# Optimization experiments

Hardware: AMD Instinct MI355X
Metric: run time of the kernel (lower is better)

The kernel has to match this reference:

```python
import jax, jax.numpy as jnp
import numpy as np


def setup_inputs() -> dict:
    key = jax.random.key(0)
    k1, k2, k3 = jax.random.split(key, 3)
    N, K, C, M = 16, 32768, 16, 128
    pred_boxes = jax.random.normal(k1, (N, K, 5), dtype=jnp.float32)
    pred_cls = jax.random.normal(k2, (N, K, C), dtype=jnp.float32)
    target = jax.random.uniform(k3, (N, M, 5), dtype=jnp.float32)
    return {"pred_boxes": pred_boxes, "pred_cls": pred_cls, "target": target}


def _losses(pred_boxes, pred_cls, target):
    N, K, _ = pred_boxes.shape
    M = target.shape[1]
    C = pred_cls.shape[2]
    mask = target.sum(axis=2) != 0                      # (N, M)
    maskf = mask.astype(pred_boxes.dtype)
    denom = maskf.sum()
    tboxes = target[..., 1:]                            # (N, M, 4) corners (x1,y1,x2,y2)
    tcls = target[..., 0].astype(jnp.int32)             # (N, M)
    pconf = pred_boxes[..., 4]                          # (N, K)
    pb = pred_boxes[..., :4]                            # (N, K, 4) (x, y, w, h)

    # pred corners (N, 1, K)
    p_x1 = pb[:, None, :, 0]
    p_y1 = pb[:, None, :, 1]
    p_x2 = (pb[..., 2] + pb[..., 0])[:, None, :]
    p_y2 = (pb[..., 3] + pb[..., 1])[:, None, :]
    # target corners (N, M, 1)
    t_x1 = tboxes[..., 0:1]
    t_y1 = tboxes[..., 1:2]
    t_x2 = tboxes[..., 2:3]
    t_y2 = tboxes[..., 3:4]

    ix1 = jnp.maximum(p_x1, t_x1)
    iy1 = jnp.maximum(p_y1, t_y1)
    ix2 = jnp.minimum(p_x2, t_x2)
    iy2 = jnp.minimum(p_y2, t_y2)
    inter = jnp.clip(ix2 - ix1 + 1, 0) * jnp.clip(iy2 - iy1 + 1, 0)   # (N, M, K)
    a1 = (p_x2 - p_x1 + 1) * (p_y2 - p_y1 + 1)
    a2 = (t_x2 - t_x1 + 1) * (t_y2 - t_y1 + 1)
    iou = inter / (a1 + a2 - inter + 1e-16)

    best = jnp.argmax(iou, axis=-1)                     # (N, M)
    best_idx = jnp.where(mask, best, 0)                 # masked targets keep index 0 (as torch init)

    best_pb = jnp.take_along_axis(pb, best_idx[..., None], axis=1)       # (N, M, 4)
    best_cls = jnp.take_along_axis(pred_cls, best_idx[..., None], axis=1)  # (N, M, C)
    # NOTE: faithful to original: conf gather indices are never updated -> always index 0
    conf_idx = jnp.zeros((N, M), dtype=jnp.int32)
    best_conf = jax.nn.sigmoid(jnp.take_along_axis(pconf, conf_idx, axis=1))  # (N, M)

    def masked_mean(v):
        return (v * maskf).sum() / denom

    logp = jax.nn.log_softmax(best_cls, axis=-1)
    ce = -jnp.take_along_axis(logp, tcls[..., None], axis=-1)[..., 0]
    loss_cls = masked_mean(ce)

    loss_x = masked_mean((best_pb[..., 0] - tboxes[..., 0]) ** 2)
    loss_y = masked_mean((best_pb[..., 1] - tboxes[..., 1]) ** 2)
    loss_w = masked_mean((best_pb[..., 2] - (tboxes[..., 2] - tboxes[..., 0])) ** 2)
    loss_h = masked_mean((best_pb[..., 3] - (tboxes[..., 3] - tboxes[..., 1])) ** 2)

    labels = (best_conf > 0.5).astype(best_conf.dtype)
    bce = -(labels * jnp.log(best_conf) + (1.0 - labels) * jnp.log(1.0 - best_conf))
    loss_conf = masked_mean(bce)

    loss = loss_cls + loss_x + loss_y + loss_w + loss_h + loss_conf
    return loss, loss_cls, loss_x, loss_y, loss_w, loss_h, loss_conf


def reference(pred_boxes, pred_cls, target):
    return _losses(pred_boxes, pred_cls, target)
```

## Files before the change

kernel.cpp:

```cpp
#include <hip/hip_runtime.h>
#include <math.h>

constexpr int N_ = 16;
constexpr int K_ = 32768;
constexpr int C_ = 16;
constexpr int M_ = 128;

constexpr int KC = 256;
constexpr int CHUNKS = K_ / KC;
constexpr int WAVES = 4;
constexpr int KSL = KC / WAVES;
constexpr int GROUPS = 16;

#define POISON_U 0xAAAAAAAAu

__device__ __forceinline__ unsigned long long load_agent_u64(
    const unsigned long long* p) {
  return __hip_atomic_load(p, __ATOMIC_RELAXED, __HIP_MEMORY_SCOPE_AGENT);
}
__device__ __forceinline__ void store_agent_f32(float* p, float v) {
  __hip_atomic_store(p, v, __ATOMIC_RELAXED, __HIP_MEMORY_SCOPE_AGENT);
}
__device__ __forceinline__ float load_agent_f32(const float* p) {
  return __hip_atomic_load(p, __ATOMIC_RELAXED, __HIP_MEMORY_SCOPE_AGENT);
}

__global__ __launch_bounds__(256, 8) void fused_loss_kernel(
    const float* __restrict__ pred_boxes,
    const float* __restrict__ pred_cls,
    const float* __restrict__ target,
    unsigned long long* __restrict__ rowmin,
    float* __restrict__ ws2,
    int* __restrict__ cnt,
    float* __restrict__ out) {
  __shared__ float4 lds4[KC];
  __shared__ float piou_s[WAVES][M_];
  __shared__ int pidx_s[WAVES][M_];
  __shared__ float red[4][7];
  __shared__ int s_flag;

  const int chunk = blockIdx.x;
  const int n = blockIdx.y;
  const int k0 = chunk * KC;
  const int tid = threadIdx.x;

  {
    const float* p = pred_boxes + ((size_t)(n * K_ + k0 + tid)) * 5;
    const float x = p[0];
    const float y = p[1];
    const float bw = p[2];
    const float bh = p[3];
    lds4[tid] = make_float4(x, y, bw + x + 1.0f, bh + y + 1.0f);
  }
  __syncthreads();

  const int wv = tid >> 6;
  const int lane = tid & 63;

  const float* tgA = target + ((size_t)(n * M_ + lane)) * 5;
  const float tx1A = tgA[1];
  const float ty1A = tgA[2];
  const float tx2A = tgA[3] + 1.0f;
  const float ty2A = tgA[4] + 1.0f;
  const float a2A = (tgA[3] - tgA[1] + 1.0f) * (tgA[4] - tgA[2] + 1.0f) + 1e-16f;

  const float* tgB = target + ((size_t)(n * M_ + lane + 64)) * 5;
  const float tx1B = tgB[1];
  const float ty1B = tgB[2];
  const float tx2B = tgB[3] + 1.0f;
  const float ty2B = tgB[4] + 1.0f;
  const float a2B = (tgB[3] - tgB[1] + 1.0f) * (tgB[4] - tgB[2] + 1.0f) + 1e-16f;

  float bestA = -INFINITY, bestB = -INFINITY;
  int bkA = 0, bkB = 0;

  const int ks = wv * KSL;
  const int ke = ks + KSL;
#pragma unroll 4
  for (int kl = ks; kl < ke; ++kl) {
    const float4 v = lds4[kl];
    const float a1 = (v.z - v.x) * (v.w - v.y);
    {
      float ww = fminf(v.z, tx2A) - fmaxf(v.x, tx1A);
      float hh = fminf(v.w, ty2A) - fmaxf(v.y, ty1A);
      ww = fmaxf(ww, 0.0f);
      hh = fmaxf(hh, 0.0f);
      const float inter = ww * hh;
      const float iou = inter * __builtin_amdgcn_rcpf((a1 + a2A) - inter);
      const bool gt = iou > bestA;
      bestA = gt ? iou : bestA;
      bkA = gt ? kl : bkA;
    }
    {
      float ww = fminf(v.z, tx2B) - fmaxf(v.x, tx1B);
      float hh = fminf(v.w, ty2B) - fmaxf(v.y, ty1B);
      ww = fmaxf(ww, 0.0f);
      hh = fmaxf(hh, 0.0f);
      const float inter = ww * hh;
      const float iou = inter * __builtin_amdgcn_rcpf((a1 + a2B) - inter);
      const bool gt = iou > bestB;
      bestB = gt ? iou : bestB;
      bkB = gt ? kl : bkB;
    }
  }

  piou_s[wv][lane] = bestA;
  pidx_s[wv][lane] = bkA;
  piou_s[wv][lane + 64] = bestB;
  pidx_s[wv][lane + 64] = bkB;
  __syncthreads();

  if (tid < M_) {
    float b = piou_s[0][tid];
    int bi = pidx_s[0][tid];
#pragma unroll
    for (int w2 = 1; w2 < WAVES; ++w2) {
      const float v = piou_s[w2][tid];
      const int id = pidx_s[w2][tid];
      const bool gt = v > b;
      b = gt ? v : b;
      bi = gt ? id : bi;
    }
    const unsigned kb = __float_as_uint(b);
    const unsigned ord = kb ^ (unsigned)(((int)kb >> 31) | 0x80000000);
    const int grp = chunk & (GROUPS - 1);
    atomicMin(&rowmin[((size_t)grp * N_ + n) * M_ + tid],
              ((unsigned long long)(~ord) << 32) | (unsigned)(k0 + bi));
  }

  __syncthreads();
  if (tid == 0) {
    const unsigned old = (unsigned)atomicAdd(&cnt[n], 1);
    s_flag = (old == POISON_U + (CHUNKS - 1)) || (old == CHUNKS - 1);
  }
  __syncthreads();
  if (!s_flag) return;

  {
    const int m = tid & (M_ - 1);
    float acc[7] = {0, 0, 0, 0, 0, 0, 0};
    if (tid < M_) {
      unsigned long long best = ~0ull;
#pragma unroll
      for (int g = 0; g < GROUPS; ++g) {
        const unsigned long long pk =
            load_agent_u64(&rowmin[((size_t)g * N_ + n) * M_ + m]);
        best = pk < best ? pk : best;
      }
      const int bidx0 = (int)(unsigned)best;

      const float* tg2 = target + ((size_t)(n * M_ + m)) * 5;
      const float t0 = tg2[0], t1 = tg2[1], t2 = tg2[2], t3 = tg2[3],
                  t4 = tg2[4];
      const float sum5 = t0 + t1 + t2 + t3 + t4;
      const float mk = (sum5 != 0.0f) ? 1.0f : 0.0f;
      const int bidx = (sum5 != 0.0f) ? bidx0 : 0;

      const float* pb = pred_boxes + ((size_t)(n * K_ + bidx)) * 5;
      const float b0 = pb[0], b1 = pb[1], bw = pb[2], bh = pb[3];

      const float4* pc =
          (const float4*)(pred_cls + ((size_t)(n * K_ + bidx)) * C_);
      float vals[C_];
#pragma unroll
      for (int q = 0; q < 4; ++q) {
        const float4 vv = pc[q];
        vals[q * 4 + 0] = vv.x;
        vals[q * 4 + 1] = vv.y;
        vals[q * 4 + 2] = vv.z;
        vals[q * 4 + 3] = vv.w;
      }
      int tcls = (int)t0;
      tcls = tcls < 0 ? 0 : (tcls >= C_ ? C_ - 1 : tcls);
      float mx = -INFINITY;
#pragma unroll
      for (int q = 0; q < C_; ++q) mx = fmaxf(mx, vals[q]);
      float se = 0.0f;
#pragma unroll
      for (int q = 0; q < C_; ++q) se += expf(vals[q] - mx);
      const float ce2 = logf(se) + mx - vals[tcls];

      const float dx = b0 - t1;
      const float dy = b1 - t2;
      const float dw = bw - (t3 - t1);
      const float dh = bh - (t4 - t2);

      const float pcf = pred_boxes[(size_t)n * K_ * 5 + 4];
      const float bc = 1.0f / (1.0f + expf(-pcf));
      const float bce = (bc > 0.5f) ? -logf(bc) : -logf(1.0f - bc);

      acc[0] = mk;
      acc[1] = mk * ce2;
      acc[2] = mk * dx * dx;
      acc[3] = mk * dy * dy;
      acc[4] = mk * dw * dw;
      acc[5] = mk * dh * dh;
      acc[6] = mk * bce;
    }

#pragma unroll
    for (int i = 0; i < 7; ++i) {
      float v = acc[i];
      for (int off = 32; off > 0; off >>= 1) v += __shfl_down(v, off, 64);
      acc[i] = v;
    }
    const int lane2 = tid & 63;
    const int wid = tid >> 6;
    if (lane2 == 0) {
#pragma unroll
      for (int i = 0; i < 7; ++i) red[wid][i] = acc[i];
    }
    __syncthreads();

    if (tid == 0) {
#pragma unroll
      for (int i = 0; i < 7; ++i)
        store_agent_f32(&ws2[n * 8 + i],
                        red[0][i] + red[1][i] + red[2][i] + red[3][i]);
    }
    __syncthreads();
    if (tid == 0) {
      const unsigned old2 = (unsigned)atomicAdd(&cnt[N_], 1);
      s_flag = (old2 == POISON_U + (N_ - 1)) || (old2 == N_ - 1);
    }
    __syncthreads();
  }

  if (s_flag && tid == 0) {
    float s[7] = {0, 0, 0, 0, 0, 0, 0};
    for (int nn = 0; nn < N_; ++nn)
#pragma unroll
      for (int i = 0; i < 7; ++i) s[i] += load_agent_f32(&ws2[nn * 8 + i]);
    const float denom = s[0];
    const float lc = s[1] / denom;
    const float lx = s[2] / denom;
    const float ly = s[3] / denom;
    const float lw = s[4] / denom;
    const float lh = s[5] / denom;
    const float lf = s[6] / denom;
    out[0] = lc + lx + ly + lw + lh + lf;
    out[1] = lc;
    out[2] = lx;
    out[3] = ly;
    out[4] = lw;
    out[5] = lh;
    out[6] = lf;
  }
}

extern "C" void kernel_launch(void* const* d_in, const int* in_sizes, int n_in,
                              void* d_out, int out_size, void* d_ws, size_t ws_size,
                              hipStream_t stream) {
  const float* pred_boxes = (const float*)d_in[0];
  const float* pred_cls = (const float*)d_in[1];
  const float* target = (const float*)d_in[2];
  float* out = (float*)d_out;

  unsigned long long* rowmin = (unsigned long long*)d_ws;
  float* ws2 = (float*)(rowmin + (size_t)GROUPS * N_ * M_);
  int* cnt = (int*)(ws2 + N_ * 8);

  dim3 g(CHUNKS, N_);
  fused_loss_kernel<<<g, 256, 0, stream>>>(pred_boxes, pred_cls, target,
                                           rowmin, ws2, cnt, out);
}
```

Before: 121.8 us.

## Pack IoU and index into single int key for max-based argmax

Packs the truncated IoU float bits with an inverted local index into a single integer so the per-iteration argmax becomes one integer max instead of a compare plus two selects. The cross-wave merge is done the same way, with the wave id folded into the low byte. It also precomputes each prediction's area into shared memory so the inner loop no longer recomputes it. Truncating the low mantissa bits of the IoU can change which index wins when IoUs are nearly equal, and the signed-int ordering of negative IoU bits can differ from float ordering.

```diff
diff --git a/kernel.cpp b/kernel.cpp
--- a/kernel.cpp
+++ b/kernel.cpp
@@ -34,8 +34,8 @@
     int* __restrict__ cnt,
     float* __restrict__ out) {
   __shared__ float4 lds4[KC];
-  __shared__ float piou_s[WAVES][M_];
-  __shared__ int pidx_s[WAVES][M_];
+  __shared__ float ldsa1[KC];
+  __shared__ int key_s[WAVES][M_];
   __shared__ float red[4][7];
   __shared__ int s_flag;
 
@@ -50,7 +50,10 @@
     const float y = p[1];
     const float bw = p[2];
     const float bh = p[3];
-    lds4[tid] = make_float4(x, y, bw + x + 1.0f, bh + y + 1.0f);
+    const float px2 = bw + x;
+    const float py2 = bh + y;
+    lds4[tid] = make_float4(x, y, px2 + 1.0f, py2 + 1.0f);
+    ldsa1[tid] = (px2 - x + 1.0f) * (py2 - y + 1.0f);
   }
   __syncthreads();
 
@@ -71,15 +74,15 @@
   const float ty2B = tgB[4] + 1.0f;
   const float a2B = (tgB[3] - tgB[1] + 1.0f) * (tgB[4] - tgB[2] + 1.0f) + 1e-16f;
 
-  float bestA = -INFINITY, bestB = -INFINITY;
-  int bkA = 0, bkB = 0;
+  int bestA = (int)0x80000000;
+  int bestB = (int)0x80000000;
 
   const int ks = wv * KSL;
-  const int ke = ks + KSL;
-#pragma unroll 4
-  for (int kl = ks; kl < ke; ++kl) {
-    const float4 v = lds4[kl];
-    const float a1 = (v.z - v.x) * (v.w - v.y);
+#pragma unroll 8
+  for (int kl = 0; kl < KSL; ++kl) {
+    const float4 v = lds4[ks + kl];
+    const float a1 = ldsa1[ks + kl];
+    const unsigned idx6 = (unsigned)(KSL - 1 - kl);
     {
       float ww = fminf(v.z, tx2A) - fmaxf(v.x, tx1A);
       float hh = fminf(v.w, ty2A) - fmaxf(v.y, ty1A);
@@ -87,9 +90,9 @@
       hh = fmaxf(hh, 0.0f);
       const float inter = ww * hh;
       const float iou = inter * __builtin_amdgcn_rcpf((a1 + a2A) - inter);
-      const bool gt = iou > bestA;
-      bestA = gt ? iou : bestA;
-      bkA = gt ? kl : bkA;
+      const int key =
+          (int)((__float_as_uint(iou) & 0xFFFFFFC0u) | idx6);
+      bestA = bestA > key ? bestA : key;
     }
     {
       float ww = fminf(v.z, tx2B) - fmaxf(v.x, tx1B);
@@ -98,34 +101,34 @@
       hh = fmaxf(hh, 0.0f);
       const float inter = ww * hh;
       const float iou = inter * __builtin_amdgcn_rcpf((a1 + a2B) - inter);
-      const bool gt = iou > bestB;
-      bestB = gt ? iou : bestB;
-      bkB = gt ? kl : bkB;
-    }
-  }
-
-  piou_s[wv][lane] = bestA;
-  pidx_s[wv][lane] = bkA;
-  piou_s[wv][lane + 64] = bestB;
-  pidx_s[wv][lane + 64] = bkB;
+      const int key = (int)((__float_as_uint(iou) & 0xFFFFFFC0u) | idx6);
+      bestB = bestB > key ? bestB : key;
+    }
+  }
+
+  {
+    const unsigned wvf = (unsigned)(3 - wv) << 6;
+    const unsigned ua = (unsigned)bestA;
+    key_s[wv][lane] = (int)((ua & 0xFFFFFF00u) | wvf | (ua & 63u));
+    const unsigned ub = (unsigned)bestB;
+    key_s[wv][lane + 64] = (int)((ub & 0xFFFFFF00u) | wvf | (ub & 63u));
+  }
   __syncthreads();
 
   if (tid < M_) {
-    float b = piou_s[0][tid];
-    int bi = pidx_s[0][tid];
+    int mg = key_s[0][tid];
 #pragma unroll
     for (int w2 = 1; w2 < WAVES; ++w2) {
-      const float v = piou_s[w2][tid];
-      const int id = pidx_s[w2][tid];
-      const bool gt = v > b;
-      b = gt ? v : b;
-      bi = gt ? id : bi;
-    }
-    const unsigned kb = __float_as_uint(b);
-    const unsigned ord = kb ^ (unsigned)(((int)kb >> 31) | 0x80000000);
+      const int v = key_s[w2][tid];
+      mg = mg > v ? mg : v;
+    }
+    const unsigned e = (unsigned)mg & 255u;
+    const int gk = k0 + (255 - (int)e);
+    const unsigned tr = (unsigned)mg & 0xFFFFFF00u;
+    const unsigned ord = tr ^ (unsigned)(((int)tr >> 31) | 0x80000000);
     const int grp = chunk & (GROUPS - 1);
     atomicMin(&rowmin[((size_t)grp * N_ + n) * M_ + tid],
-              ((unsigned long long)(~ord) << 32) | (unsigned)(k0 + bi));
+              ((unsigned long long)(~ord) << 32) | (unsigned)gk);
   }
 
   __syncthreads();
```

Result: faster. 116.4 us (-4.5%).
